# Optimization experiments

Measured on AMD Instinct MI355X. Metric: run time of the kernel, lower is better.

## Reference

```python
import jax, jax.numpy as jnp
import numpy as np

B, C, H, W = 32, 64, 128, 128

def setup_inputs() -> dict:
    key = jax.random.key(0)
    k1, k2, k3, k4 = jax.random.split(key, 4)
    x = jax.random.normal(k1, (B, C, H, W), dtype=jnp.float32)
    theta = jax.random.normal(k2, (C, C), dtype=jnp.float32) * (6.0 / (C + C)) ** 0.5  # xavier-ish
    W_lin = jax.random.normal(k3, (C, C), dtype=jnp.float32) * (1.0 / C) ** 0.5
    b_lin = jax.random.normal(k4, (C,), dtype=jnp.float32) * 0.01
    return {"x": x, "theta": theta, "W_lin": W_lin, "b_lin": b_lin}

def reference(x, theta, W_lin, b_lin):
    b, c, h, w = x.shape
    # channel descriptor: global average pool -> [B, C]
    wvec = jnp.mean(x, axis=(2, 3))
    # pairwise diff and soft adjacency, batched over B
    diff = wvec[:, :, None] - wvec[:, None, :]              # [B, C, C]
    e = jnp.exp(-diff)
    T = jnp.abs(1.0 - e / (1.0 + e)) - 1.0                  # [B, C, C]
    A = 0.5 * (T + jnp.swapaxes(T, 1, 2)) * theta           # [B, C, C]
    # graph conv: A @ x_flat, relu
    x_flat = x.reshape(b, c, h * w)                         # [B, C, HW]
    Hmat = jax.nn.relu(jnp.einsum('bij,bjn->bin', A, x_flat))  # [B, C, HW]
    # Linear over channel dim applied to H.T: [B, HW, C]
    Hout = jnp.einsum('bin,ci->bnc', Hmat, W_lin) + b_lin   # [B, HW, C]
    # faithful to torch: H.view(C, h, w) is a raw row-major reshape of [HW, C]
    return Hout.reshape(b, c, h, w)
```

## Files before the change

kernel.cpp:

```cpp
#include <hip/hip_runtime.h>

static constexpr int Cc  = 64;
static constexpr int HWc = 16384;
static constexpr int Bc  = 32;


typedef _Float16 v8h __attribute__((ext_vector_type(8)));
typedef float    v4f __attribute__((ext_vector_type(4)));

union FragU { uint32_t u[4]; v8h h; };

__device__ inline uint32_t packf2(float lo, float hi) {
  union { _Float16 h[2]; uint32_t u; } r;
  r.h[0] = (_Float16)lo; r.h[1] = (_Float16)hi;
  return r.u;
}

__device__ inline v4f mfma16(v8h a, v8h b, v4f c) {
  return __builtin_amdgcn_mfma_f32_16x16x32_f16(a, b, c, 0, 0, 0);
}

__global__ void prep_weights(const float* __restrict__ theta,
                             const float* __restrict__ Wlin,
                             _Float16* __restrict__ M1h,
                             _Float16* __restrict__ Wh) {
  int t = blockIdx.x * 256 + threadIdx.x;
  if (t < Cc * Cc) {
    M1h[t] = (_Float16)(-0.5f * theta[t]);
    Wh[t]  = (_Float16)(Wlin[t]);
  }
}

__global__ __launch_bounds__(256, 4) void fused_mfma(
    const float* __restrict__ x,
    const _Float16* __restrict__ M1h,
    const _Float16* __restrict__ Wh,
    const float* __restrict__ blin,
    float* __restrict__ out)
{
  __shared__ __align__(16) uint32_t xp[4][32][36];
  __shared__ __align__(16) _Float16 p2[4][16][72];
  __shared__ __align__(16) _Float16 w2l[64][72];

  const int tid  = threadIdx.x;
  const int wv   = tid >> 6;
  const int l    = tid & 63;
  const int lq   = tid & 15;
  const int quad = l >> 4;

  const int b     = blockIdx.x >> 5;
  const int npix0 = (blockIdx.x & 31) * 512 + wv * 128;
  const float* xb = x + (size_t)b * Cc * HWc + npix0;

  {
    const int r = tid >> 2, seg = (tid & 3) * 16;
    const uint4* wg = (const uint4*)(Wh + r * 64 + seg);
    uint4 a0 = wg[0], a1 = wg[1];
    *(uint4*)&w2l[r][seg]     = a0;
    *(uint4*)&w2l[r][seg + 8] = a1;
  }

  const v8h* M1v = (const v8h*)M1h;
  v8h w1[4][2];
#pragma unroll
  for (int it = 0; it < 4; ++it)
#pragma unroll
    for (int kt = 0; kt < 2; ++kt)
      w1[it][kt] = M1v[(it * 16 + lq) * 8 + kt * 4 + quad];
  v4f bias4[4];
#pragma unroll
  for (int ct = 0; ct < 4; ++ct)
    bias4[ct] = *(const v4f*)(blin + ct * 16 + quad * 4);

  const int sp_ = l >> 3;
  const int sc  = (l & 7) * 4;

#pragma unroll
  for (int rep = 0; rep < 4; ++rep) {
    const int p = rep * 8 + sp_;
    const float4 e = *(const float4*)(xb + (size_t)(2 * p)     * HWc + sc);
    const float4 o = *(const float4*)(xb + (size_t)(2 * p + 1) * HWc + sc);
    uint4 w;
    w.x = packf2(e.x, o.x); w.y = packf2(e.y, o.y);
    w.z = packf2(e.z, o.z); w.w = packf2(e.w, o.w);
    *(uint4*)&xp[wv][p][sc] = w;
  }

  __syncthreads();

#pragma unroll
  for (int t = 0; t < 4; ++t) {
    float4 pf[8];
    if (t < 3) {
      const float* xt = xb + (t + 1) * 32;
#pragma unroll
      for (int rep = 0; rep < 4; ++rep) {
        const int p = rep * 8 + sp_;
        pf[2 * rep]     = *(const float4*)(xt + (size_t)(2 * p)     * HWc + sc);
        pf[2 * rep + 1] = *(const float4*)(xt + (size_t)(2 * p + 1) * HWc + sc);
      }
    }

#pragma unroll
    for (int nt = 0; nt < 2; ++nt) {
      FragU xf[2];
#pragma unroll
      for (int kt = 0; kt < 2; ++kt)
#pragma unroll
        for (int r = 0; r < 4; ++r)
          xf[kt].u[r] = xp[wv][kt * 16 + quad * 4 + r][nt * 16 + lq];

#pragma unroll
      for (int it = 0; it < 4; ++it) {
        v4f a = {0.f, 0.f, 0.f, 0.f};
#pragma unroll
        for (int kt = 0; kt < 2; ++kt)
          a = mfma16(w1[it][kt], xf[kt].h, a);
        uint2 w;
        w.x = packf2(fmaxf(a[0], 0.f), fmaxf(a[1], 0.f));
        w.y = packf2(fmaxf(a[2], 0.f), fmaxf(a[3], 0.f));
        *(uint2*)&p2[wv][lq][it * 16 + quad * 4] = w;
      }

      FragU pr[2];
#pragma unroll
      for (int kt = 0; kt < 2; ++kt)
        pr[kt].h = *(const v8h*)&p2[wv][lq][kt * 32 + quad * 8];

      float* orow = out + ((size_t)b * HWc + npix0 + t * 32 + nt * 16 + lq) * Cc
                    + quad * 4;
#pragma unroll
      for (int ct = 0; ct < 4; ++ct) {
        v4f a = bias4[ct];
#pragma unroll
        for (int kt = 0; kt < 2; ++kt) {
          const v8h b2 = *(const v8h*)&w2l[ct * 16 + lq][kt * 32 + quad * 8];
          a = mfma16(b2, pr[kt].h, a);
        }
        *(v4f*)(orow + ct * 16) = a;
      }
    }

    if (t < 3) {
#pragma unroll
      for (int rep = 0; rep < 4; ++rep) {
        const int p = rep * 8 + sp_;
        uint4 w;
        w.x = packf2(pf[2 * rep].x, pf[2 * rep + 1].x);
        w.y = packf2(pf[2 * rep].y, pf[2 * rep + 1].y);
        w.z = packf2(pf[2 * rep].z, pf[2 * rep + 1].z);
        w.w = packf2(pf[2 * rep].w, pf[2 * rep + 1].w);
        *(uint4*)&xp[wv][p][sc] = w;
      }
    }
  }
}

extern "C" void kernel_launch(void* const* d_in, const int* in_sizes, int n_in,
                              void* d_out, int out_size, void* d_ws, size_t ws_size,
                              hipStream_t stream) {
  const float* x     = (const float*)d_in[0];
  const float* theta = (const float*)d_in[1];
  const float* W_lin = (const float*)d_in[2];
  const float* b_lin = (const float*)d_in[3];
  float* out = (float*)d_out;

  _Float16* M1h = (_Float16*)d_ws;
  _Float16* Wh  = M1h + Cc * Cc;

  prep_weights<<<(Cc * Cc + 255) / 256, 256, 0, stream>>>(theta, W_lin, M1h, Wh);

  const int nblocks = Bc * HWc / 512;
  fused_mfma<<<nblocks, 256, 0, stream>>>(x, M1h, Wh, b_lin, out);
}
```

Before: 249.0 us.

## Stream x tiles into LDS via async global_load_lds and hold W_lin in registers

Replaces the register-staged prefetch, in which fp32 loads were packed to fp16 and written to LDS, with direct global-to-LDS DMA loads (global_load_lds) into a per-wave fp32 buffer. The fp16 packing now happens after the LDS read. The second-stage weight matrix moves from shared memory into registers, the block-wide __syncthreads is dropped because each wave owns its own tile, and output stores become nontemporal. The aim is to cut VGPR pressure and LDS traffic and to overlap the next tile's fetch with compute. In exchange, occupancy is lowered to 3 blocks per CU, and correctness depends on the compiler inserting the right vmcnt waits for the DMA writes.

Result: no change. 251.1 us (+0.8%).

```diff
diff --git a/kernel.cpp b/kernel.cpp
--- a/kernel.cpp
+++ b/kernel.cpp
@@ -3,6 +3,8 @@
 static constexpr int Cc  = 64;
 static constexpr int HWc = 16384;
 static constexpr int Bc  = 32;
+static constexpr int TPX = 32;
+static constexpr int TT  = 4;
 
 
 typedef _Float16 v8h __attribute__((ext_vector_type(8)));
@@ -20,6 +22,12 @@
   return __builtin_amdgcn_mfma_f32_16x16x32_f16(a, b, c, 0, 0, 0);
 }
 
+__device__ inline void gload_lds16(const float* g, float* l) {
+  __builtin_amdgcn_global_load_lds(
+      (const __attribute__((address_space(1))) void*)g,
+      (__attribute__((address_space(3))) void*)l, 16, 0, 0);
+}
+
 __global__ void prep_weights(const float* __restrict__ theta,
                              const float* __restrict__ Wlin,
                              _Float16* __restrict__ M1h,
@@ -31,16 +39,15 @@
   }
 }
 
-__global__ __launch_bounds__(256, 4) void fused_mfma(
+__global__ __launch_bounds__(256, 3) void fused_mfma(
     const float* __restrict__ x,
     const _Float16* __restrict__ M1h,
     const _Float16* __restrict__ Wh,
     const float* __restrict__ blin,
     float* __restrict__ out)
 {
-  __shared__ __align__(16) uint32_t xp[4][32][36];
-  __shared__ __align__(16) _Float16 p2[4][16][72];
-  __shared__ __align__(16) _Float16 w2l[64][72];
+  __shared__ __align__(16) float    xa[4][64][32];
+  __shared__ __align__(16) _Float16 p2[4][32][80];
 
   const int tid  = threadIdx.x;
   const int wv   = tid >> 6;
@@ -49,56 +56,54 @@
   const int quad = l >> 4;
 
   const int b     = blockIdx.x >> 5;
-  const int npix0 = (blockIdx.x & 31) * 512 + wv * 128;
-  const float* xb = x + (size_t)b * Cc * HWc + npix0;
+  const int npix0 = (blockIdx.x & 31) * 512 + wv * (TT * TPX);
+  const float* xb = x + (size_t)b * Cc * HWc;
 
-  {
-    const int r = tid >> 2, seg = (tid & 3) * 16;
-    const uint4* wg = (const uint4*)(Wh + r * 64 + seg);
-    uint4 a0 = wg[0], a1 = wg[1];
-    *(uint4*)&w2l[r][seg]     = a0;
-    *(uint4*)&w2l[r][seg + 8] = a1;
-  }
+  const int gch = l >> 3;
+  const int gpx = (l & 7) * 4;
 
   const v8h* M1v = (const v8h*)M1h;
-  v8h w1[4][2];
+  const v8h* Whv = (const v8h*)Wh;
+  v8h w1[4][2], w2[4][2];
 #pragma unroll
   for (int it = 0; it < 4; ++it)
 #pragma unroll
-    for (int kt = 0; kt < 2; ++kt)
+    for (int kt = 0; kt < 2; ++kt) {
       w1[it][kt] = M1v[(it * 16 + lq) * 8 + kt * 4 + quad];
+      w2[it][kt] = Whv[(it * 16 + lq) * 8 + kt * 4 + quad];
+    }
   v4f bias4[4];
 #pragma unroll
   for (int ct = 0; ct < 4; ++ct)
     bias4[ct] = *(const v4f*)(blin + ct * 16 + quad * 4);
 
-  const int sp_ = l >> 3;
-  const int sc  = (l & 7) * 4;
+#pragma unroll
+  for (int i = 0; i < 8; ++i)
+    gload_lds16(xb + (size_t)(i * 8 + gch) * HWc + npix0 + gpx, &xa[wv][i * 8][0]);
 
 #pragma unroll
-  for (int rep = 0; rep < 4; ++rep) {
-    const int p = rep * 8 + sp_;
-    const float4 e = *(const float4*)(xb + (size_t)(2 * p)     * HWc + sc);
-    const float4 o = *(const float4*)(xb + (size_t)(2 * p + 1) * HWc + sc);
-    uint4 w;
-    w.x = packf2(e.x, o.x); w.y = packf2(e.y, o.y);
-    w.z = packf2(e.z, o.z); w.w = packf2(e.w, o.w);
-    *(uint4*)&xp[wv][p][sc] = w;
-  }
+  for (int t = 0; t < TT; ++t) {
+    const int n0 = npix0 + t * TPX;
 
-  __syncthreads();
+    float f[2][2][4][2];
+#pragma unroll
+    for (int nt = 0; nt < 2; ++nt)
+#pragma unroll
+      for (int kt = 0; kt < 2; ++kt)
+#pragma unroll
+        for (int r = 0; r < 4; ++r) {
+          const int c = kt * 16 + quad * 4 + r;
+          f[nt][kt][r][0] = xa[wv][2 * c][nt * 16 + lq];
+          f[nt][kt][r][1] = xa[wv][2 * c + 1][nt * 16 + lq];
+        }
+    asm volatile("s_waitcnt lgkmcnt(0)" ::: "memory");
+    __builtin_amdgcn_sched_barrier(0);
 
+    if (t + 1 < TT) {
 #pragma unroll
-  for (int t = 0; t < 4; ++t) {
-    float4 pf[8];
-    if (t < 3) {
-      const float* xt = xb + (t + 1) * 32;
-#pragma unroll
-      for (int rep = 0; rep < 4; ++rep) {
-        const int p = rep * 8 + sp_;
-        pf[2 * rep]     = *(const float4*)(xt + (size_t)(2 * p)     * HWc + sc);
-        pf[2 * rep + 1] = *(const float4*)(xt + (size_t)(2 * p + 1) * HWc + sc);
-      }
+      for (int i = 0; i < 8; ++i)
+        gload_lds16(xb + (size_t)(i * 8 + gch) * HWc + n0 + TPX + gpx,
+                    &xa[wv][i * 8][0]);
     }
 
 #pragma unroll
@@ -108,49 +113,30 @@
       for (int kt = 0; kt < 2; ++kt)
 #pragma unroll
         for (int r = 0; r < 4; ++r)
-          xf[kt].u[r] = xp[wv][kt * 16 + quad * 4 + r][nt * 16 + lq];
+          xf[kt].u[r] = packf2(f[nt][kt][r][0], f[nt][kt][r][1]);
 
 #pragma unroll
       for (int it = 0; it < 4; ++it) {
         v4f a = {0.f, 0.f, 0.f, 0.f};
-#pragma unroll
-        for (int kt = 0; kt < 2; ++kt)
-          a = mfma16(w1[it][kt], xf[kt].h, a);
+        a = mfma16(w1[it][0], xf[0].h, a);
+        a = mfma16(w1[it][1], xf[1].h, a);
         uint2 w;
         w.x = packf2(fmaxf(a[0], 0.f), fmaxf(a[1], 0.f));
         w.y = packf2(fmaxf(a[2], 0.f), fmaxf(a[3], 0.f));
-        *(uint2*)&p2[wv][lq][it * 16 + quad * 4] = w;
+        *(uint2*)&p2[wv][nt * 16 + lq][it * 16 + quad * 4] = w;
       }
 
       FragU pr[2];
-#pragma unroll
-      for (int kt = 0; kt < 2; ++kt)
-        pr[kt].h = *(const v8h*)&p2[wv][lq][kt * 32 + quad * 8];
+      pr[0].h = *(const v8h*)&p2[wv][nt * 16 + lq][quad * 8];
+      pr[1].h = *(const v8h*)&p2[wv][nt * 16 + lq][32 + quad * 8];
 
-      float* orow = out + ((size_t)b * HWc + npix0 + t * 32 + nt * 16 + lq) * Cc
-                    + quad * 4;
+      float* orow = out + ((size_t)b * HWc + n0 + nt * 16 + lq) * Cc + quad * 4;
 #pragma unroll
       for (int ct = 0; ct < 4; ++ct) {
         v4f a = bias4[ct];
-#pragma unroll
-        for (int kt = 0; kt < 2; ++kt) {
-          const v8h b2 = *(const v8h*)&w2l[ct * 16 + lq][kt * 32 + quad * 8];
-          a = mfma16(b2, pr[kt].h, a);
-        }
-        *(v4f*)(orow + ct * 16) = a;
-      }
-    }
-
-    if (t < 3) {
-#pragma unroll
-      for (int rep = 0; rep < 4; ++rep) {
-        const int p = rep * 8 + sp_;
-        uint4 w;
-        w.x = packf2(pf[2 * rep].x, pf[2 * rep + 1].x);
-        w.y = packf2(pf[2 * rep].y, pf[2 * rep + 1].y);
-        w.z = packf2(pf[2 * rep].z, pf[2 * rep + 1].z);
-        w.w = packf2(pf[2 * rep].w, pf[2 * rep + 1].w);
-        *(uint4*)&xp[wv][p][sc] = w;
+        a = mfma16(w2[ct][0], pr[0].h, a);
+        a = mfma16(w2[ct][1], pr[1].h, a);
+        __builtin_nontemporal_store(a, (v4f*)(orow + ct * 16));
       }
     }
   }
```
